# Kernel optimization log

Hardware: AMD Instinct MI355X
Metric: run time of the kernel (lower is better)

Reference implementation:

```python
import jax, jax.numpy as jnp
import numpy as np

B, N, DX, DE, DY = 256, 128, 8, 5, 4
NEG = 1e9
TEMP_CONST = 0.5


def encode_no_edge(E):
    # set class 0 where the one-hot row is all-zero, then zero the diagonal
    no_edge = jnp.sum(E, axis=-1) == 0
    first = jnp.where(no_edge, 1.0, E[..., 0])
    E = jnp.concatenate([first[..., None], E[..., 1:]], axis=-1)
    n = E.shape[1]
    return E * (1.0 - jnp.eye(n, dtype=E.dtype))[None, :, :, None]


def _disc(X, E, y, node_mask, wx, we, wy):
    # simple discriminator head: masked mean-pool + linear -> one logit per graph
    nm = node_mask.astype(X.dtype)
    pair = nm[:, :, None] * nm[:, None, :]
    xm = jnp.mean(X * nm[..., None], axis=1)          # [B, DX+1]
    em = jnp.mean(E * pair[..., None], axis=(1, 2))   # [B, DE+1]
    return xm @ wx + em @ we + y @ wy                 # [B]


def setup_inputs():
    key = jax.random.key(0)
    ks = jax.random.split(key, 12)
    Xc = jax.random.randint(ks[0], (B, N), 0, DX + 1)  # class DX == masked
    X = jax.nn.one_hot(Xc, DX + 1, dtype=jnp.float32)
    r = jax.random.randint(ks[1], (B, N, N), 0, DE + 1)  # class DE == masked
    r = jnp.triu(r, 1)
    Ec = r + jnp.swapaxes(r, 1, 2)
    E = encode_no_edge(jax.nn.one_hot(Ec, DE + 1, dtype=jnp.float32))
    y = jax.random.normal(ks[2], (B, DY), dtype=jnp.float32)
    node_mask = jnp.ones((B, N), dtype=bool)
    logits_x = jax.random.normal(ks[3], (B, N, DX), dtype=jnp.float32)
    logits_e = jax.random.normal(ks[4], (B, N, N, DE), dtype=jnp.float32)

    def gumbel(k, shape):
        u = jax.random.uniform(k, shape, minval=1e-6, maxval=1.0 - 1e-6)
        return -jnp.log(-jnp.log(u))

    g_edge = gumbel(ks[5], (B, N, N))
    g_node = gumbel(ks[6], (B, N))
    g_cat_e = gumbel(ks[7], (B, N, N, DE))
    g_cat_x = gumbel(ks[8], (B, N, DX))
    wx = 0.1 * jax.random.normal(ks[9], (DX + 1,), dtype=jnp.float32)
    we = 0.1 * jax.random.normal(ks[10], (DE + 1,), dtype=jnp.float32)
    wy = 0.1 * jax.random.normal(ks[11], (DY,), dtype=jnp.float32)
    return {"X": X, "E": E, "y": y, "node_mask": node_mask,
            "logits_x": logits_x, "logits_e": logits_e,
            "g_edge": g_edge, "g_node": g_node,
            "g_cat_e": g_cat_e, "g_cat_x": g_cat_x,
            "wx": wx, "we": we, "wy": wy, "step_size": 1}


def reference(X, E, y, node_mask, logits_x, logits_e, g_edge, g_node,
              g_cat_e, g_cat_x, wx, we, wy, step_size):
    b, n = X.shape[0], X.shape[1]
    dx, de = logits_x.shape[-1], logits_e.shape[-1]
    nm = node_mask.astype(X.dtype)
    pair = nm[:, :, None] * nm[:, None, :]
    triu = jnp.triu(jnp.ones((n, n), dtype=bool), 1)[None]

    # tempering exponent (get_temp_exponent, from current X, E)
    Xc0 = jnp.argmax(X, axis=-1)
    Ec0 = jnp.argmax(E, axis=-1)
    num_nodes = jnp.sum(nm, axis=-1)
    num_elem = num_nodes + num_nodes * (num_nodes - 1) / 2
    masked_n = jnp.sum((Xc0 == dx) & node_mask, axis=-1)
    masked_e = jnp.sum((Ec0 == de) & triu & (pair > 0), axis=(-1, -2))
    temp = TEMP_CONST * (1.0 - (masked_n + masked_e) / num_elem)

    # ---------------- unmask edges ----------------
    Eclass = Ec0
    absorbed_e = (Eclass == de) & triu & (pair > 0)
    k_e = jnp.minimum(jnp.sum(absorbed_e, axis=(-1, -2)), step_size)
    lg = (g_edge - (~absorbed_e) * NEG).reshape(b, -1)
    ranks = jnp.argsort(jnp.argsort(-lg, axis=-1), axis=-1)
    unmask_e = (ranks < k_e[:, None]).reshape(b, n, n)
    w_e = jnp.ones((b, n, n, de), X.dtype)
    for i in range(de):
        Ec = jnp.where(unmask_e, i, Eclass)
        Ec = jnp.triu(Ec, 1)
        Ec = Ec + jnp.swapaxes(Ec, 1, 2)
        E_new = encode_no_edge(jax.nn.one_hot(Ec, de + 1, dtype=X.dtype))
        d = _disc(X, E_new, y, node_mask, wx, we, wy) * temp
        w_e = w_e.at[..., i].set(jnp.where(unmask_e, jnp.exp(d)[:, None, None], 1.0))
        Eclass = Ec
    guided_e = jax.nn.softmax(logits_e, axis=-1) * w_e
    pred_e = jnp.argmax(jnp.log(guided_e + 1e-30) + g_cat_e, axis=-1)  # multinomial via Gumbel-max
    Ec = jnp.where(unmask_e, pred_e, Eclass)
    Ec = jnp.triu(Ec, 1)
    Ec = Ec + jnp.swapaxes(Ec, 1, 2)
    E_out = encode_no_edge(jax.nn.one_hot(Ec, de + 1, dtype=X.dtype))

    # ---------------- unmask nodes (uses original E, as in forward_step) ----------------
    absorbed_n = (Xc0 == dx) & node_mask
    k_n = jnp.minimum(jnp.sum(absorbed_n, axis=-1), step_size)
    lgn = g_node - (~absorbed_n) * NEG
    ranks_n = jnp.argsort(jnp.argsort(-lgn, axis=-1), axis=-1)
    unmask_n = ranks_n < k_n[:, None]
    Xclass = Xc0
    w_x = jnp.ones((b, n, dx), X.dtype)
    for i in range(dx):
        Xc = jnp.where(unmask_n, i, Xclass)
        X_new = jax.nn.one_hot(Xc, dx + 1, dtype=X.dtype)
        d = _disc(X_new, E, y, node_mask, wx, we, wy) * temp
        w_x = w_x.at[..., i].set(jnp.where(unmask_n, jnp.exp(d)[:, None], 1.0))
        Xclass = Xc
    guided_x = jax.nn.softmax(logits_x, axis=-1) * w_x
    pred_x = jnp.argmax(jnp.log(guided_x + 1e-30) + g_cat_x, axis=-1)
    Xc = jnp.where(unmask_n, pred_x, Xclass)
    X_out = jax.nn.one_hot(Xc, dx + 1, dtype=X.dtype)

    # PlaceHolder.mask(node_mask)
    X_out = X_out * nm[..., None]
    E_out = E_out * pair[..., None]
    return X_out, E_out
```

## Files before the change

kernel.cpp:

```cpp
#include <hip/hip_runtime.h>
#include <math.h>


struct Part { float we_sum; int me_cnt; float best_ge; int best_ei; };

__global__ __launch_bounds__(256) void ardg_e_pass(
    const float* __restrict__ E, const float* __restrict__ Ge,
    const float* __restrict__ wep, float* __restrict__ outE,
    Part* __restrict__ ws)
{
    const int blk = blockIdx.x;
    const int b   = blk >> 3;
    const int sub = blk & 7;
    const int tid = threadIdx.x;

    const float we0 = wep[0], we1 = wep[1], we2 = wep[2],
                we3 = wep[3], we4 = wep[4], we5 = wep[5];

    const size_t ebase = (size_t)b * 98304;
    const float4* __restrict__ Ein = (const float4*)(E + ebase);
    float4* __restrict__ Eo4       = (float4*)(outE + ebase);
    const float* __restrict__ geb  = Ge + (size_t)b * 16384;

    float we_sum  = 0.f;
    int   me_cnt  = 0;
    float best_ge = -1e30f;
    int   best_ei = 0x3fffffff;

    #pragma unroll
    for (int k = 0; k < 4; ++k) {
        const int g = (sub << 10) + tid + (k << 8);
        const float4 va = Ein[3*g+0];
        const float4 vb = Ein[3*g+1];
        const float4 vc = Ein[3*g+2];
        Eo4[3*g+0] = va; Eo4[3*g+1] = vb; Eo4[3*g+2] = vc;
        const int i0 = 2*g, i1 = 2*g + 1;
        {
            float m = va.x; int c = 0;
            if (va.y > m) { m = va.y; c = 1; }
            if (va.z > m) { m = va.z; c = 2; }
            if (va.w > m) { m = va.w; c = 3; }
            if (vb.x > m) { m = vb.x; c = 4; }
            if (vb.y > m) { m = vb.y; c = 5; }
            const int p = i0 >> 7, q = i0 & 127;
            if (p != q) {
                we_sum += (c==0?we0:c==1?we1:c==2?we2:c==3?we3:c==4?we4:we5);
                if (p < q && c == 5) {
                    me_cnt++;
                    const float gg = geb[i0];
                    if (gg > best_ge) { best_ge = gg; best_ei = i0; }
                }
            }
        }
        {
            float m = vb.z; int c = 0;
            if (vb.w > m) { m = vb.w; c = 1; }
            if (vc.x > m) { m = vc.x; c = 2; }
            if (vc.y > m) { m = vc.y; c = 3; }
            if (vc.z > m) { m = vc.z; c = 4; }
            if (vc.w > m) { m = vc.w; c = 5; }
            const int p = i1 >> 7, q = i1 & 127;
            if (p != q) {
                we_sum += (c==0?we0:c==1?we1:c==2?we2:c==3?we3:c==4?we4:we5);
                if (p < q && c == 5) {
                    me_cnt++;
                    const float gg = geb[i1];
                    if (gg > best_ge) { best_ge = gg; best_ei = i1; }
                }
            }
        }
    }

    __shared__ float sf[256];
    __shared__ int   si[256];

    sf[tid] = we_sum; __syncthreads();
    for (int s = 128; s > 0; s >>= 1) { if (tid < s) sf[tid] += sf[tid+s]; __syncthreads(); }
    const float S_we = sf[0]; __syncthreads();

    si[tid] = me_cnt; __syncthreads();
    for (int s = 128; s > 0; s >>= 1) { if (tid < s) si[tid] += si[tid+s]; __syncthreads(); }
    const int ME = si[0]; __syncthreads();

    sf[tid] = best_ge; si[tid] = best_ei; __syncthreads();
    for (int s = 128; s > 0; s >>= 1) {
        if (tid < s) {
            const float v = sf[tid+s]; const int ix = si[tid+s];
            if (v > sf[tid] || (v == sf[tid] && ix < si[tid])) { sf[tid] = v; si[tid] = ix; }
        }
        __syncthreads();
    }

    if (tid == 0) {
        Part p; p.we_sum = S_we; p.me_cnt = ME; p.best_ge = sf[0]; p.best_ei = si[0];
        ws[blk] = p;
    }
}

__global__ __launch_bounds__(128) void ardg_finalize(
    const float* __restrict__ X, const float* __restrict__ Y,
    const float* __restrict__ Lx, const float* __restrict__ Le,
    const float* __restrict__ Gn, const float* __restrict__ Gce,
    const float* __restrict__ Gcx, const float* __restrict__ wxp,
    const float* __restrict__ wep, const float* __restrict__ wyp,
    const int* __restrict__ stepp, const Part* __restrict__ ws,
    float* __restrict__ outX, float* __restrict__ outE)
{
    const int b   = blockIdx.x;
    const int tid = threadIdx.x;

    const float wv0=wxp[0],wv1=wxp[1],wv2=wxp[2],wv3=wxp[3],wv4=wxp[4],
                wv5=wxp[5],wv6=wxp[6],wv7=wxp[7],wv8=wxp[8];

    const float* xr = X    + ((size_t)b * 128 + tid) * 9;
    float*       xo = outX + ((size_t)b * 128 + tid) * 9;
    const float x0=xr[0],x1=xr[1],x2=xr[2],x3=xr[3],x4=xr[4],
                x5=xr[5],x6=xr[6],x7=xr[7],x8=xr[8];
    xo[0]=x0;xo[1]=x1;xo[2]=x2;xo[3]=x3;xo[4]=x4;
    xo[5]=x5;xo[6]=x6;xo[7]=x7;xo[8]=x8;
    float m = x0; int c = 0;
    if (x1>m){m=x1;c=1;} if (x2>m){m=x2;c=2;} if (x3>m){m=x3;c=3;}
    if (x4>m){m=x4;c=4;} if (x5>m){m=x5;c=5;} if (x6>m){m=x6;c=6;}
    if (x7>m){m=x7;c=7;} if (x8>m){m=x8;c=8;}
    float wx_sum = (c==0?wv0:c==1?wv1:c==2?wv2:c==3?wv3:c==4?wv4:
                    c==5?wv5:c==6?wv6:c==7?wv7:wv8);
    int   mn_cnt  = 0;
    float best_gn = -1e30f;
    int   best_ni = 0x3fffffff;
    if (c == 8) {
        mn_cnt  = 1;
        best_gn = Gn[(size_t)b * 128 + tid];
        best_ni = tid;
    }

    __shared__ float sf[128];
    __shared__ int   si[128];

    sf[tid] = wx_sum; __syncthreads();
    for (int s = 64; s > 0; s >>= 1) { if (tid < s) sf[tid] += sf[tid+s]; __syncthreads(); }
    const float S_wx = sf[0]; __syncthreads();

    si[tid] = mn_cnt; __syncthreads();
    for (int s = 64; s > 0; s >>= 1) { if (tid < s) si[tid] += si[tid+s]; __syncthreads(); }
    const int MN = si[0]; __syncthreads();

    sf[tid] = best_gn; si[tid] = best_ni; __syncthreads();
    for (int s = 64; s > 0; s >>= 1) {
        if (tid < s) {
            const float v = sf[tid+s]; const int ix = si[tid+s];
            if (v > sf[tid] || (v == sf[tid] && ix < si[tid])) { sf[tid] = v; si[tid] = ix; }
        }
        __syncthreads();
    }
    const int NIDX = si[0];

    if (tid == 0) {
        float S_we = 0.f; int ME = 0; float bge = -1e30f; int EIDX = 0x3fffffff;
        #pragma unroll
        for (int s = 0; s < 8; ++s) {
            const Part p = ws[b*8 + s];
            S_we += p.we_sum; ME += p.me_cnt;
            if (p.best_ge > bge || (p.best_ge == bge && p.best_ei < EIDX)) {
                bge = p.best_ge; EIDX = p.best_ei;
            }
        }

        const float we0 = wep[0], we1 = wep[1], we2 = wep[2],
                    we3 = wep[3], we4 = wep[4], we5 = wep[5];
        const float temp = 0.5f * (1.0f - (float)(ME + MN) / 8256.0f);
        const double yw = (double)Y[b*4+0]*(double)wyp[0] + (double)Y[b*4+1]*(double)wyp[1]
                        + (double)Y[b*4+2]*(double)wyp[2] + (double)Y[b*4+3]*(double)wyp[3];
        const int step = stepp[0];
        const double xmwx = (double)S_wx / 128.0;
        const double emwe = (double)S_we / 16384.0;
        const size_t ebase = (size_t)b * 98304;

        if (ME > 0 && step > 0) {
            const int ei = EIDX;
            const int p = ei >> 7, q = ei & 127;
            const float* le = Le  + ((size_t)b*16384 + ei)*5;
            const float* gc = Gce + ((size_t)b*16384 + ei)*5;
            const float l0=le[0],l1=le[1],l2=le[2],l3=le[3],l4=le[4];
            const float lm = fmaxf(fmaxf(fmaxf(l0,l1),fmaxf(l2,l3)),l4);
            const float e0=expf(l0-lm),e1=expf(l1-lm),e2=expf(l2-lm),
                        e3=expf(l3-lm),e4=expf(l4-lm);
            const float es = e0+e1+e2+e3+e4;
            const float pv[5]  = {e0,e1,e2,e3,e4};
            const float wev[5] = {we0,we1,we2,we3,we4};
            const float gcv[5] = {gc[0],gc[1],gc[2],gc[3],gc[4]};
            const double basee = xmwx + yw + ((double)S_we - 2.0*(double)we5) / 16384.0;
            double bsc = -1e300; int pe = 0;
            for (int i = 0; i < 5; ++i) {
                const double d  = (double)temp * (basee + 2.0*(double)wev[i] / 16384.0);
                const double sc = log((double)(pv[i]/es) * exp(d) + 1e-30) + (double)gcv[i];
                if (sc > bsc) { bsc = sc; pe = i; }
            }
            float* r1 = outE + ebase + (size_t)ei * 6;
            float* r2 = outE + ebase + (size_t)(q*128 + p) * 6;
            for (int cc = 0; cc < 6; ++cc) {
                const float v = (cc == pe) ? 1.0f : 0.0f;
                r1[cc] = v; r2[cc] = v;
            }
        }

        if (MN > 0 && step > 0) {
            const int ni = NIDX;
            const float* lxr = Lx  + ((size_t)b*128 + ni)*8;
            const float* gcx = Gcx + ((size_t)b*128 + ni)*8;
            float l[8], ev[8];
            float lm = -1e30f;
            for (int i = 0; i < 8; ++i) { l[i] = lxr[i]; lm = fmaxf(lm, l[i]); }
            float es = 0.f;
            for (int i = 0; i < 8; ++i) { ev[i] = expf(l[i]-lm); es += ev[i]; }
            const float wxv[8] = {wv0,wv1,wv2,wv3,wv4,wv5,wv6,wv7};
            double bsc = -1e300; int px = 0;
            for (int i = 0; i < 8; ++i) {
                const double d  = (double)temp *
                    ( ((double)S_wx - (double)wv8 + (double)wxv[i]) / 128.0 + yw + emwe );
                const double sc = log((double)(ev[i]/es) * exp(d) + 1e-30) + (double)gcx[i];
                if (sc > bsc) { bsc = sc; px = i; }
            }
            float* r = outX + ((size_t)b*128 + ni)*9;
            for (int cc = 0; cc < 9; ++cc) r[cc] = (cc == px) ? 1.0f : 0.0f;
        }
    }
}

extern "C" void kernel_launch(void* const* d_in, const int* in_sizes, int n_in,
                              void* d_out, int out_size, void* d_ws, size_t ws_size,
                              hipStream_t stream) {
    const float* X   = (const float*)d_in[0];
    const float* E   = (const float*)d_in[1];
    const float* Y   = (const float*)d_in[2];
    const float* Lx  = (const float*)d_in[4];
    const float* Le  = (const float*)d_in[5];
    const float* Ge  = (const float*)d_in[6];
    const float* Gn  = (const float*)d_in[7];
    const float* Gce = (const float*)d_in[8];
    const float* Gcx = (const float*)d_in[9];
    const float* wx  = (const float*)d_in[10];
    const float* we  = (const float*)d_in[11];
    const float* wy  = (const float*)d_in[12];
    const int*   st  = (const int*)d_in[13];

    float* outX = (float*)d_out;
    float* outE = (float*)d_out + (size_t)256 * 128 * 9;
    Part*  ws   = (Part*)d_ws;

    hipLaunchKernelGGL(ardg_e_pass, dim3(2048), dim3(256), 0, stream,
                       E, Ge, we, outE, ws);
    hipLaunchKernelGGL(ardg_finalize, dim3(256), dim3(128), 0, stream,
                       X, Y, Lx, Le, Gn, Gce, Gcx, wx, we, wy, st, ws,
                       outX, outE);
}
```

Baseline: 54.86 us.

## Fuse edge pass and finalize into one kernel using last-block atomic counter

Merges the two kernels into one: each of the 8 sub-blocks per graph reduces its partial edge sums, then bumps an atomic counter, and the last block to arrive runs the per-graph finalize (node reductions, unmasking, output patching). The edge loop is also restructured to 192 threads with coalesced float4 loads batched 8 at a time. It replaces the per-edge argmax with a dot product against a per-lane rotated weight vector, relying on one-hot rows. This removes a second kernel launch and the gap between kernels, at the cost of a memset, atomics/fences, and the assumption that E and X are exactly one-hot.

```diff
diff --git a/kernel.cpp b/kernel.cpp
--- a/kernel.cpp
+++ b/kernel.cpp
@@ -4,15 +4,23 @@
 
 struct Part { float we_sum; int me_cnt; float best_ge; int best_ei; };
 
-__global__ __launch_bounds__(256) void ardg_e_pass(
-    const float* __restrict__ E, const float* __restrict__ Ge,
-    const float* __restrict__ wep, float* __restrict__ outE,
-    Part* __restrict__ ws)
+__global__ __launch_bounds__(192) void ardg_all(
+    const float* __restrict__ X, const float* __restrict__ E,
+    const float* __restrict__ Y, const float* __restrict__ Lx,
+    const float* __restrict__ Le, const float* __restrict__ Ge,
+    const float* __restrict__ Gn, const float* __restrict__ Gce,
+    const float* __restrict__ Gcx, const float* __restrict__ wxp,
+    const float* __restrict__ wep, const float* __restrict__ wyp,
+    const int* __restrict__ stepp,
+    float* __restrict__ outX, float* __restrict__ outE,
+    Part* __restrict__ parts, int* __restrict__ counters)
 {
     const int blk = blockIdx.x;
     const int b   = blk >> 3;
     const int sub = blk & 7;
     const int tid = threadIdx.x;
+    const int l   = tid & 63;
+    const int w   = tid >> 6;
 
     const float we0 = wep[0], we1 = wep[1], we2 = wep[2],
                 we3 = wep[3], we4 = wep[4], we5 = wep[5];
@@ -22,50 +30,44 @@
     float4* __restrict__ Eo4       = (float4*)(outE + ebase);
     const float* __restrict__ geb  = Ge + (size_t)b * 16384;
 
-    float we_sum  = 0.f;
-    int   me_cnt  = 0;
-    float best_ge = -1e30f;
-    int   best_ei = 0x3fffffff;
-
+    const int c = (w + l) % 3;
+    const float4 W =
+        (c == 0) ? make_float4(we0, we1, we2, we3) :
+        (c == 1) ? make_float4(we4, we5, we0, we1) :
+                   make_float4(we2, we3, we4, we5);
+
+    const unsigned Jbase = sub * 3072u + w * 64u + (unsigned)l;
+
+    float wsum = 0.f;
+    int   me   = 0;
+    float bge  = -1e30f;
+    int   bei  = 0x3fffffff;
+
+    float4 d[8];
     #pragma unroll
-    for (int k = 0; k < 4; ++k) {
-        const int g = (sub << 10) + tid + (k << 8);
-        const float4 va = Ein[3*g+0];
-        const float4 vb = Ein[3*g+1];
-        const float4 vc = Ein[3*g+2];
-        Eo4[3*g+0] = va; Eo4[3*g+1] = vb; Eo4[3*g+2] = vc;
-        const int i0 = 2*g, i1 = 2*g + 1;
-        {
-            float m = va.x; int c = 0;
-            if (va.y > m) { m = va.y; c = 1; }
-            if (va.z > m) { m = va.z; c = 2; }
-            if (va.w > m) { m = va.w; c = 3; }
-            if (vb.x > m) { m = vb.x; c = 4; }
-            if (vb.y > m) { m = vb.y; c = 5; }
-            const int p = i0 >> 7, q = i0 & 127;
-            if (p != q) {
-                we_sum += (c==0?we0:c==1?we1:c==2?we2:c==3?we3:c==4?we4:we5);
-                if (p < q && c == 5) {
-                    me_cnt++;
-                    const float gg = geb[i0];
-                    if (gg > best_ge) { best_ge = gg; best_ei = i0; }
-                }
-            }
-        }
-        {
-            float m = vb.z; int c = 0;
-            if (vb.w > m) { m = vb.w; c = 1; }
-            if (vc.x > m) { m = vc.x; c = 2; }
-            if (vc.y > m) { m = vc.y; c = 3; }
-            if (vc.z > m) { m = vc.z; c = 4; }
-            if (vc.w > m) { m = vc.w; c = 5; }
-            const int p = i1 >> 7, q = i1 & 127;
-            if (p != q) {
-                we_sum += (c==0?we0:c==1?we1:c==2?we2:c==3?we3:c==4?we4:we5);
-                if (p < q && c == 5) {
-                    me_cnt++;
-                    const float gg = geb[i1];
-                    if (gg > best_ge) { best_ge = gg; best_ei = i1; }
+    for (int half = 0; half < 2; ++half) {
+        #pragma unroll
+        for (int j = 0; j < 8; ++j)
+            d[j] = Ein[Jbase + (half * 8 + j) * 192u];
+        #pragma unroll
+        for (int j = 0; j < 8; ++j) {
+            const unsigned J = Jbase + (half * 8 + j) * 192u;
+            Eo4[J] = d[j];
+            wsum = fmaf(d[j].x, W.x, wsum);
+            wsum = fmaf(d[j].y, W.y, wsum);
+            wsum = fmaf(d[j].z, W.z, wsum);
+            wsum = fmaf(d[j].w, W.w, wsum);
+            if (c) {
+                const float val = (c == 1) ? d[j].y : d[j].w;
+                if (val > 0.5f) {
+                    const unsigned pair = (c == 1) ? (2u*J - 2u) / 3u
+                                                   : (2u*J - 1u) / 3u;
+                    const int p = pair >> 7, q = pair & 127;
+                    if (p < q) {
+                        me++;
+                        const float g = geb[pair];
+                        if (g > bge) { bge = g; bei = (int)pair; }
+                    }
                 }
             }
         }
@@ -73,16 +75,21 @@
 
     __shared__ float sf[256];
     __shared__ int   si[256];
-
-    sf[tid] = we_sum; __syncthreads();
+    __shared__ int   sWin;
+
+    sf[tid] = wsum; if (tid < 64) sf[192 + tid] = 0.f;
+    __syncthreads();
     for (int s = 128; s > 0; s >>= 1) { if (tid < s) sf[tid] += sf[tid+s]; __syncthreads(); }
-    const float S_we = sf[0]; __syncthreads();
-
-    si[tid] = me_cnt; __syncthreads();
+    const float S_we_p = sf[0]; __syncthreads();
+
+    si[tid] = me; if (tid < 64) si[192 + tid] = 0;
+    __syncthreads();
     for (int s = 128; s > 0; s >>= 1) { if (tid < s) si[tid] += si[tid+s]; __syncthreads(); }
-    const int ME = si[0]; __syncthreads();
-
-    sf[tid] = best_ge; si[tid] = best_ei; __syncthreads();
+    const int ME_p = si[0]; __syncthreads();
+
+    sf[tid] = bge; si[tid] = bei;
+    if (tid < 64) { sf[192 + tid] = -1e30f; si[192 + tid] = 0x3fffffff; }
+    __syncthreads();
     for (int s = 128; s > 0; s >>= 1) {
         if (tid < s) {
             const float v = sf[tid+s]; const int ix = si[tid+s];
@@ -92,60 +99,51 @@
     }
 
     if (tid == 0) {
-        Part p; p.we_sum = S_we; p.me_cnt = ME; p.best_ge = sf[0]; p.best_ei = si[0];
-        ws[blk] = p;
-    }
-}
-
-__global__ __launch_bounds__(128) void ardg_finalize(
-    const float* __restrict__ X, const float* __restrict__ Y,
-    const float* __restrict__ Lx, const float* __restrict__ Le,
-    const float* __restrict__ Gn, const float* __restrict__ Gce,
-    const float* __restrict__ Gcx, const float* __restrict__ wxp,
-    const float* __restrict__ wep, const float* __restrict__ wyp,
-    const int* __restrict__ stepp, const Part* __restrict__ ws,
-    float* __restrict__ outX, float* __restrict__ outE)
-{
-    const int b   = blockIdx.x;
-    const int tid = threadIdx.x;
+        Part p; p.we_sum = S_we_p; p.me_cnt = ME_p; p.best_ge = sf[0]; p.best_ei = si[0];
+        parts[blk] = p;
+        __threadfence();
+        const int old = atomicAdd(&counters[b], 1);
+        sWin = (old == 7);
+    }
+    __syncthreads();
+    if (!sWin) return;
+
+    if (tid == 0) __threadfence();
+
+    const float4* Xi4 = (const float4*)(X    + (size_t)b * 1152);
+    float4*       Xo4 = (float4*)      (outX + (size_t)b * 1152);
+    for (int j = tid; j < 288; j += 192) Xo4[j] = Xi4[j];
 
     const float wv0=wxp[0],wv1=wxp[1],wv2=wxp[2],wv3=wxp[3],wv4=wxp[4],
                 wv5=wxp[5],wv6=wxp[6],wv7=wxp[7],wv8=wxp[8];
 
-    const float* xr = X    + ((size_t)b * 128 + tid) * 9;
-    float*       xo = outX + ((size_t)b * 128 + tid) * 9;
-    const float x0=xr[0],x1=xr[1],x2=xr[2],x3=xr[3],x4=xr[4],
-                x5=xr[5],x6=xr[6],x7=xr[7],x8=xr[8];
-    xo[0]=x0;xo[1]=x1;xo[2]=x2;xo[3]=x3;xo[4]=x4;
-    xo[5]=x5;xo[6]=x6;xo[7]=x7;xo[8]=x8;
-    float m = x0; int c = 0;
-    if (x1>m){m=x1;c=1;} if (x2>m){m=x2;c=2;} if (x3>m){m=x3;c=3;}
-    if (x4>m){m=x4;c=4;} if (x5>m){m=x5;c=5;} if (x6>m){m=x6;c=6;}
-    if (x7>m){m=x7;c=7;} if (x8>m){m=x8;c=8;}
-    float wx_sum = (c==0?wv0:c==1?wv1:c==2?wv2:c==3?wv3:c==4?wv4:
-                    c==5?wv5:c==6?wv6:c==7?wv7:wv8);
-    int   mn_cnt  = 0;
-    float best_gn = -1e30f;
-    int   best_ni = 0x3fffffff;
-    if (c == 8) {
-        mn_cnt  = 1;
-        best_gn = Gn[(size_t)b * 128 + tid];
-        best_ni = tid;
-    }
-
-    __shared__ float sf[128];
-    __shared__ int   si[128];
-
-    sf[tid] = wx_sum; __syncthreads();
-    for (int s = 64; s > 0; s >>= 1) { if (tid < s) sf[tid] += sf[tid+s]; __syncthreads(); }
+    float wx_sum = 0.f;
+    int   mn     = 0;
+    float bgn    = -1e30f;
+    int   bni    = 0x3fffffff;
+    if (tid < 128) {
+        const float* xr = X + ((size_t)b * 128 + tid) * 9;
+        const float x0=xr[0],x1=xr[1],x2=xr[2],x3=xr[3],x4=xr[4],
+                    x5=xr[5],x6=xr[6],x7=xr[7],x8=xr[8];
+        wx_sum = x0*wv0+x1*wv1+x2*wv2+x3*wv3+x4*wv4+x5*wv5+x6*wv6+x7*wv7+x8*wv8;
+        if (x8 > 0.5f) { mn = 1; bgn = Gn[(size_t)b*128 + tid]; bni = tid; }
+    }
+    __syncthreads();
+
+    sf[tid] = wx_sum; if (tid < 64) sf[192 + tid] = 0.f;
+    __syncthreads();
+    for (int s = 128; s > 0; s >>= 1) { if (tid < s) sf[tid] += sf[tid+s]; __syncthreads(); }
     const float S_wx = sf[0]; __syncthreads();
 
-    si[tid] = mn_cnt; __syncthreads();
-    for (int s = 64; s > 0; s >>= 1) { if (tid < s) si[tid] += si[tid+s]; __syncthreads(); }
+    si[tid] = mn; if (tid < 64) si[192 + tid] = 0;
+    __syncthreads();
+    for (int s = 128; s > 0; s >>= 1) { if (tid < s) si[tid] += si[tid+s]; __syncthreads(); }
     const int MN = si[0]; __syncthreads();
 
-    sf[tid] = best_gn; si[tid] = best_ni; __syncthreads();
-    for (int s = 64; s > 0; s >>= 1) {
+    sf[tid] = bgn; si[tid] = bni;
+    if (tid < 64) { sf[192 + tid] = -1e30f; si[192 + tid] = 0x3fffffff; }
+    __syncthreads();
+    for (int s = 128; s > 0; s >>= 1) {
         if (tid < s) {
             const float v = sf[tid+s]; const int ix = si[tid+s];
             if (v > sf[tid] || (v == sf[tid] && ix < si[tid])) { sf[tid] = v; si[tid] = ix; }
@@ -155,25 +153,25 @@
     const int NIDX = si[0];
 
     if (tid == 0) {
-        float S_we = 0.f; int ME = 0; float bge = -1e30f; int EIDX = 0x3fffffff;
+        float S_we = 0.f; int ME = 0; float bg = -1e30f; int EIDX = 0x3fffffff;
         #pragma unroll
         for (int s = 0; s < 8; ++s) {
-            const Part p = ws[b*8 + s];
-            S_we += p.we_sum; ME += p.me_cnt;
-            if (p.best_ge > bge || (p.best_ge == bge && p.best_ei < EIDX)) {
-                bge = p.best_ge; EIDX = p.best_ei;
-            }
-        }
-
-        const float we0 = wep[0], we1 = wep[1], we2 = wep[2],
-                    we3 = wep[3], we4 = wep[4], we5 = wep[5];
+            const int* pw = (const int*)(parts + b*8 + s);
+            const int i0 = __hip_atomic_load(pw+0, __ATOMIC_RELAXED, __HIP_MEMORY_SCOPE_AGENT);
+            const int i1 = __hip_atomic_load(pw+1, __ATOMIC_RELAXED, __HIP_MEMORY_SCOPE_AGENT);
+            const int i2 = __hip_atomic_load(pw+2, __ATOMIC_RELAXED, __HIP_MEMORY_SCOPE_AGENT);
+            const int i3 = __hip_atomic_load(pw+3, __ATOMIC_RELAXED, __HIP_MEMORY_SCOPE_AGENT);
+            S_we += __int_as_float(i0); ME += i1;
+            const float g = __int_as_float(i2);
+            if (g > bg || (g == bg && i3 < EIDX)) { bg = g; EIDX = i3; }
+        }
+
         const float temp = 0.5f * (1.0f - (float)(ME + MN) / 8256.0f);
         const double yw = (double)Y[b*4+0]*(double)wyp[0] + (double)Y[b*4+1]*(double)wyp[1]
                         + (double)Y[b*4+2]*(double)wyp[2] + (double)Y[b*4+3]*(double)wyp[3];
         const int step = stepp[0];
         const double xmwx = (double)S_wx / 128.0;
         const double emwe = (double)S_we / 16384.0;
-        const size_t ebase = (size_t)b * 98304;
 
         if (ME > 0 && step > 0) {
             const int ei = EIDX;
@@ -191,8 +189,8 @@
             const double basee = xmwx + yw + ((double)S_we - 2.0*(double)we5) / 16384.0;
             double bsc = -1e300; int pe = 0;
             for (int i = 0; i < 5; ++i) {
-                const double d  = (double)temp * (basee + 2.0*(double)wev[i] / 16384.0);
-                const double sc = log((double)(pv[i]/es) * exp(d) + 1e-30) + (double)gcv[i];
+                const double dd = (double)temp * (basee + 2.0*(double)wev[i] / 16384.0);
+                const double sc = log((double)(pv[i]/es) * exp(dd) + 1e-30) + (double)gcv[i];
                 if (sc > bsc) { bsc = sc; pe = i; }
             }
             float* r1 = outE + ebase + (size_t)ei * 6;
@@ -207,17 +205,17 @@
             const int ni = NIDX;
             const float* lxr = Lx  + ((size_t)b*128 + ni)*8;
             const float* gcx = Gcx + ((size_t)b*128 + ni)*8;
-            float l[8], ev[8];
+            float lv[8], ev[8];
             float lm = -1e30f;
-            for (int i = 0; i < 8; ++i) { l[i] = lxr[i]; lm = fmaxf(lm, l[i]); }
+            for (int i = 0; i < 8; ++i) { lv[i] = lxr[i]; lm = fmaxf(lm, lv[i]); }
             float es = 0.f;
-            for (int i = 0; i < 8; ++i) { ev[i] = expf(l[i]-lm); es += ev[i]; }
+            for (int i = 0; i < 8; ++i) { ev[i] = expf(lv[i]-lm); es += ev[i]; }
             const float wxv[8] = {wv0,wv1,wv2,wv3,wv4,wv5,wv6,wv7};
             double bsc = -1e300; int px = 0;
             for (int i = 0; i < 8; ++i) {
-                const double d  = (double)temp *
+                const double dd = (double)temp *
                     ( ((double)S_wx - (double)wv8 + (double)wxv[i]) / 128.0 + yw + emwe );
-                const double sc = log((double)(ev[i]/es) * exp(d) + 1e-30) + (double)gcx[i];
+                const double sc = log((double)(ev[i]/es) * exp(dd) + 1e-30) + (double)gcx[i];
                 if (sc > bsc) { bsc = sc; px = i; }
             }
             float* r = outX + ((size_t)b*128 + ni)*9;
@@ -245,11 +243,12 @@
 
     float* outX = (float*)d_out;
     float* outE = (float*)d_out + (size_t)256 * 128 * 9;
-    Part*  ws   = (Part*)d_ws;
-
-    hipLaunchKernelGGL(ardg_e_pass, dim3(2048), dim3(256), 0, stream,
-                       E, Ge, we, outE, ws);
-    hipLaunchKernelGGL(ardg_finalize, dim3(256), dim3(128), 0, stream,
-                       X, Y, Lx, Le, Gn, Gce, Gcx, wx, we, wy, st, ws,
-                       outX, outE);
+
+    int*  counters = (int*)d_ws;
+    Part* parts    = (Part*)((char*)d_ws + 1024);
+
+    hipMemsetAsync(d_ws, 0, 1024, stream);
+    hipLaunchKernelGGL(ardg_all, dim3(2048), dim3(192), 0, stream,
+                       X, E, Y, Lx, Le, Ge, Gn, Gce, Gcx, wx, we, wy, st,
+                       outX, outE, parts, counters);
 }
```

Result: slower. 169.4 us (+208.7%).
